# Kernel optimization log

Hardware: AMD Instinct MI355X
Metric: run time of the kernel (lower is better)

## Reference

```python
import jax, jax.numpy as jnp
import numpy as np

BN_EPS = 1e-5


def setup_inputs() -> dict:
    key = jax.random.key(0)
    ks = jax.random.split(key, 6)
    B, C, N = 8, 256, 2048
    C4 = C // 4
    return {
        "x": jax.random.normal(ks[0], (B, C, N), dtype=jnp.float32),
        "wq": jax.random.normal(ks[1], (C4, C), dtype=jnp.float32) * (1.0 / np.sqrt(C)),
        "wv": jax.random.normal(ks[2], (C, C), dtype=jnp.float32) * (1.0 / np.sqrt(C)),
        "bv": jax.random.normal(ks[3], (C,), dtype=jnp.float32) * 0.02,
        "wt": jax.random.normal(ks[4], (C, C), dtype=jnp.float32) * (1.0 / np.sqrt(C)),
        "bt": jax.random.normal(ks[5], (C,), dtype=jnp.float32) * 0.02,
        "gamma": jnp.ones((C,), dtype=jnp.float32),
        "beta": jnp.zeros((C,), dtype=jnp.float32),
    }


def reference(x, wq, wv, bv, wt, bt, gamma, beta):
    # x: [B, C, N]. Conv1d(kernel=1) == per-point matmul.
    # q_conv and k_conv share the same weight in the original, so q == k.
    q = jnp.einsum('oc,bcn->bon', wq, x)            # [B, C/4, N]
    # ||q_i - q_j||_2 via the Gram identity (same math as norm of the diff tensor)
    sq = jnp.sum(q * q, axis=1)                     # [B, N]
    gram = jnp.einsum('bci,bcj->bij', q, q)         # [B, N, N]
    d2 = sq[:, :, None] - 2.0 * gram + sq[:, None, :]
    l2 = jnp.sqrt(jnp.maximum(d2, 0.0))             # [B, N, N]
    attn = jax.nn.softmax(-l2, axis=-1)             # rows = queries i
    v = jnp.einsum('oc,bcn->bon', wv, x) + bv[None, :, None]   # [B, C, N]
    # einsum('bij,bkj->bik') then permute(0,2,1) == contract j directly to [B, C, N]
    x_r = jnp.einsum('bij,bcj->bci', attn, v)       # [B, C, N]
    t = jnp.einsum('oc,bcn->bon', wt, x_r) + bt[None, :, None]
    # BatchNorm1d in training mode: batch stats over (B, N), biased variance
    mean = jnp.mean(t, axis=(0, 2), keepdims=True)
    var = jnp.mean((t - mean) ** 2, axis=(0, 2), keepdims=True)
    bn = gamma[None, :, None] * (t - mean) * jax.lax.rsqrt(var + BN_EPS) + beta[None, :, None]
    return x + jnp.maximum(bn, 0.0)
```

## Files before the change

kernel.cpp:

```cpp
#include <hip/hip_runtime.h>
#include <math.h>

#define BDIM 8
#define CDIM 256
#define C4DIM 64
#define NDIM 2048
#define LOG2E_SQ 2.0813689810056077f
#define NEG_2LOG2E_SQ -4.1627379620112154f

typedef short bf16x8 __attribute__((ext_vector_type(8)));
typedef float f32x4 __attribute__((ext_vector_type(4)));

__device__ inline unsigned cvt_pk(float lo, float hi) {
  unsigned r;
  asm("v_cvt_pk_bf16_f32 %0, %1, %2" : "=v"(r) : "v"(lo), "v"(hi));
  return r;
}
__device__ inline float bflo(unsigned u) {
  u <<= 16; float f; __builtin_memcpy(&f, &u, 4); return f;
}
__device__ inline float bfhi(unsigned u) {
  u &= 0xffff0000u; float f; __builtin_memcpy(&f, &u, 4); return f;
}

__global__ __launch_bounds__(256) void prep_kernel(const float* __restrict__ x,
                                                   const float* __restrict__ wq,
                                                   const float* __restrict__ wv,
                                                   const float* __restrict__ wt,
                                                   short* __restrict__ xT,
                                                   short* __restrict__ xb,
                                                   short* __restrict__ wqb,
                                                   short* __restrict__ wvb,
                                                   short* __restrict__ wtb,
                                                   float* __restrict__ bnsum) {
  __shared__ float tile[64][65];
  const int fb = blockIdx.x, t = threadIdx.x;
  if (fb < 1024) {
    const int b = fb >> 7, c0 = ((fb >> 5) & 3) * 64, n0 = (fb & 31) * 64;
    const int cl = t >> 2, ng = (t & 3) * 16;
#pragma unroll
    for (int kk = 0; kk < 4; ++kk) {
      const size_t src = ((size_t)(b * CDIM + c0 + cl)) * NDIM + n0 + ng + kk * 4;
      float4 v = *(const float4*)&x[src];
      tile[cl][ng + kk * 4 + 0] = v.x; tile[cl][ng + kk * 4 + 1] = v.y;
      tile[cl][ng + kk * 4 + 2] = v.z; tile[cl][ng + kk * 4 + 3] = v.w;
      *(uint2*)&xb[src] = make_uint2(cvt_pk(v.x, v.y), cvt_pk(v.z, v.w));
    }
    __syncthreads();
    const int nl = t >> 2, cg = (t & 3) * 16;
    unsigned u[8];
#pragma unroll
    for (int e = 0; e < 8; ++e)
      u[e] = cvt_pk(tile[cg + 2 * e][nl], tile[cg + 2 * e + 1][nl]);
    short* dst = &xT[((size_t)b * NDIM + n0 + nl) * CDIM + c0 + cg];
    *(uint4*)&dst[0] = make_uint4(u[0], u[1], u[2], u[3]);
    *(uint4*)&dst[8] = make_uint4(u[4], u[5], u[6], u[7]);
  } else if (fb < 1168) {
    const int idx = ((fb - 1024) * 256 + t) * 4;
    const float* src; short* dst; int off;
    if (idx < 16384)      { src = wq; dst = wqb; off = idx; }
    else if (idx < 81920) { src = wv; dst = wvb; off = idx - 16384; }
    else                  { src = wt; dst = wtb; off = idx - 81920; }
    float4 v = *(const float4*)&src[off];
    *(uint2*)&dst[off] = make_uint2(cvt_pk(v.x, v.y), cvt_pk(v.z, v.w));
  } else {
    bnsum[t] = 0.f; bnsum[256 + t] = 0.f;
  }
}

template<bool STATS>
__device__ __forceinline__ void gemm128(const short* __restrict__ Wb,
                                        const short* __restrict__ Xt,
                                        const float* __restrict__ bias,
                                        short* __restrict__ OUT,
                                        float* __restrict__ bnsum,
                                        float* __restrict__ bnss,
                                        int b, int n0, int c0, int t) {
  const int w = t >> 6, l = t & 63, il = l & 15, g = l >> 4;
  const int wn = w & 1, wc = w >> 1;
  const size_t arow = (size_t)b * NDIM + n0 + wn * 64;
  const int ccol = c0 + wc * 64;
  f32x4 acc[4][4] = {};
#pragma unroll
  for (int ks = 0; ks < 8; ++ks) {
    const int k0 = ks * 32;
    bf16x8 af[4], bfr[4];
#pragma unroll
    for (int nt = 0; nt < 4; ++nt)
      af[nt] = *(const bf16x8*)&Xt[(arow + nt * 16 + il) * CDIM + k0 + g * 8];
#pragma unroll
    for (int ct = 0; ct < 4; ++ct)
      bfr[ct] = *(const bf16x8*)&Wb[(size_t)(ccol + ct * 16 + il) * CDIM + k0 + g * 8];
#pragma unroll
    for (int nt = 0; nt < 4; ++nt)
#pragma unroll
      for (int ct = 0; ct < 4; ++ct)
        acc[nt][ct] = __builtin_amdgcn_mfma_f32_16x16x32_bf16(af[nt], bfr[ct], acc[nt][ct], 0, 0, 0);
  }
#pragma unroll
  for (int ct = 0; ct < 4; ++ct) {
    const int c = ccol + ct * 16 + il;
    const float bs = bias[c];
    float s = 0.f, ss = 0.f;
#pragma unroll
    for (int nt = 0; nt < 4; ++nt) {
      const int n = n0 + wn * 64 + nt * 16 + g * 4;
      float y0 = acc[nt][ct][0] + bs, y1 = acc[nt][ct][1] + bs;
      float y2 = acc[nt][ct][2] + bs, y3 = acc[nt][ct][3] + bs;
      *(uint2*)&OUT[((size_t)(b * CDIM + c)) * NDIM + n] =
          make_uint2(cvt_pk(y0, y1), cvt_pk(y2, y3));
      if (STATS) {
        s += y0 + y1 + y2 + y3;
        ss += y0 * y0 + y1 * y1 + y2 * y2 + y3 * y3;
      }
    }
    if (STATS) {
      s += __shfl_xor(s, 16, 64);   s += __shfl_xor(s, 32, 64);
      ss += __shfl_xor(ss, 16, 64); ss += __shfl_xor(ss, 32, 64);
      if (l < 16) { atomicAdd(&bnsum[c], s); atomicAdd(&bnss[c], ss); }
    }
  }
}

__global__ __launch_bounds__(256) void qv_gemm(const short* __restrict__ wqb,
                                               const short* __restrict__ wvb,
                                               const short* __restrict__ xT,
                                               const float* __restrict__ bv,
                                               short* __restrict__ qT,
                                               float* __restrict__ sq2,
                                               short* __restrict__ vbf) {
  const int fb = blockIdx.x, t = threadIdx.x;
  if (fb < 256) {
    const int b = fb >> 5, c0 = ((fb >> 4) & 1) * 128, n0 = (fb & 15) * 128;
    gemm128<false>(wvb, xT, bv, vbf, nullptr, nullptr, b, n0, c0, t);
  } else {
    const int f = fb - 256;
    const int b = f >> 5, n0 = (f & 31) * 64;
    const int w = t >> 6, l = t & 63, il = l & 15, g = l >> 4;
    const int nw = n0 + w * 16;
    f32x4 acc[4] = {};
#pragma unroll
    for (int ks = 0; ks < 8; ++ks) {
      const int k0 = ks * 32;
      bf16x8 bx = *(const bf16x8*)&xT[((size_t)b * NDIM + nw + il) * CDIM + k0 + g * 8];
#pragma unroll
      for (int ot = 0; ot < 4; ++ot) {
        bf16x8 aw = *(const bf16x8*)&wqb[(size_t)(ot * 16 + il) * CDIM + k0 + g * 8];
        acc[ot] = __builtin_amdgcn_mfma_f32_16x16x32_bf16(aw, bx, acc[ot], 0, 0, 0);
      }
    }
    float sqs = 0.f;
#pragma unroll
    for (int ot = 0; ot < 4; ++ot) {
      unsigned u0 = cvt_pk(acc[ot][0], acc[ot][1]);
      unsigned u1 = cvt_pk(acc[ot][2], acc[ot][3]);
      *(uint2*)&qT[((size_t)b * NDIM + nw + il) * C4DIM + ot * 16 + g * 4] = make_uint2(u0, u1);
      float f0 = bflo(u0), f1 = bfhi(u0), f2 = bflo(u1), f3 = bfhi(u1);
      sqs += f0 * f0 + f1 * f1 + f2 * f2 + f3 * f3;
    }
    sqs += __shfl_xor(sqs, 16, 64);
    sqs += __shfl_xor(sqs, 32, 64);
    if (l < 16) sq2[(size_t)b * NDIM + nw + l] = sqs * LOG2E_SQ;
  }
}

__global__ __launch_bounds__(512) void attn_mfma(const short* __restrict__ qT,
                                                 const short* __restrict__ Vb16,
                                                 const float* __restrict__ sq2,
                                                 short* __restrict__ xrT) {
  __shared__ __align__(16) short vj[2][256 * 32];
  __shared__ __align__(16) short qj[2][32 * 64];
  __shared__ __align__(16) short wlds[2][4][16][40];
  __shared__ float sums_lds[8][16];

  const int bid = blockIdx.x;
  const int swz = (bid & 7) * 32 + (bid >> 3);
  const int i0 = (swz & 31) * 64;
  const int b  = swz >> 5;

  const int t = threadIdx.x;
  const int w = t >> 6, l = t & 63, il = l & 15, g = l >> 4;
  const int isub = w & 3, chalf = w >> 2;

  const short* qTb = qT + (size_t)b * NDIM * C4DIM;
  const short* Vbb = Vb16 + (size_t)b * CDIM * NDIM;
  const float* sqb = sq2 + (size_t)b * NDIM;

  const int iglob = i0 + isub * 16 + il;
  const bf16x8 bq0 = *(const bf16x8*)&qTb[(size_t)iglob * C4DIM + g * 8];
  const bf16x8 bq1 = *(const bf16x8*)&qTb[(size_t)iglob * C4DIM + 32 + g * 8];
  const float sqi = sqb[iglob];

  const int vcb = t >> 2, vs = t & 3;
  const int vd0 = vcb * 32 + ((vs ^ ((vcb >> 1) & 3)) << 3);
  const int vd1 = vd0 + 128 * 32;
  const int qrow = t >> 3, qslot = t & 7;
  const int qd = qrow * 64 + ((qslot ^ (qrow & 7)) << 3);

  f32x4 acc[8];
#pragma unroll
  for (int k = 0; k < 8; ++k) acc[k] = {0.f, 0.f, 0.f, 0.f};
  float sumw = 0.f;

  f32x4 sqc;
  {
    if (t < 256) {
      bf16x8 qr = *(const bf16x8*)&qTb[(size_t)qrow * C4DIM + qslot * 8];
      *(bf16x8*)&qj[0][qd] = qr;
    }
    sqc = *(const f32x4*)&sqb[chalf * 16 + g * 4];
  }
  __syncthreads();

  const int NT = NDIM / 32;
  for (int jt = 0; jt <= NT; ++jt) {
    const int p = jt & 1;
    const bool dg = (jt < NT);
    const bool dp = (jt > 0);
    const bool nq = (jt + 1 < NT);

    bf16x8 vr0 = {}, vr1 = {}, qr = {};
    f32x4 tn = {};
    if (dg) {
      const int j0 = jt * 32;
      vr0 = *(const bf16x8*)&Vbb[(size_t)vcb * NDIM + j0 + vs * 8];
      vr1 = *(const bf16x8*)&Vbb[(size_t)(vcb + 128) * NDIM + j0 + vs * 8];
    }
    if (nq) {
      const int j1 = (jt + 1) * 32;
      if (t < 256) qr = *(const bf16x8*)&qTb[(size_t)(j1 + qrow) * C4DIM + qslot * 8];
      tn = *(const f32x4*)&sqb[j1 + chalf * 16 + g * 4];
    }

    f32x4 s = {0.f, 0.f, 0.f, 0.f};
    if (dg) {
      const short* qbuf = &qj[p][0];
      const int row = chalf * 16 + il;
      bf16x8 aJ0 = *(const bf16x8*)&qbuf[row * 64 + ((g ^ (il & 7)) << 3)];
      bf16x8 aJ1 = *(const bf16x8*)&qbuf[row * 64 + (((4 + g) ^ (il & 7)) << 3)];
      s = __builtin_amdgcn_mfma_f32_16x16x32_bf16(aJ0, bq0, s, 0, 0, 0);
      s = __builtin_amdgcn_mfma_f32_16x16x32_bf16(aJ1, bq1, s, 0, 0, 0);
    }

    if (dp) {
      const int pp = p ^ 1;
      const short* vbuf = &vj[pp][0];
      const bf16x8 bw = *(const bf16x8*)&wlds[pp][isub][il][g * 8];
      __builtin_amdgcn_s_setprio(1);
#pragma unroll
      for (int ctl = 0; ctl < 8; ++ctl) {
        const int lr = chalf * 128 + ctl * 16 + il;
        bf16x8 aV = *(const bf16x8*)&vbuf[lr * 32 + ((g ^ ((il >> 1) & 3)) << 3)];
        acc[ctl] = __builtin_amdgcn_mfma_f32_16x16x32_bf16(aV, bw, acc[ctl], 0, 0, 0);
      }
      __builtin_amdgcn_s_setprio(0);
    }

    if (dg) {
      float wv[4];
#pragma unroll
      for (int r = 0; r < 4; ++r) {
        float e = fmaxf(fmaf(NEG_2LOG2E_SQ, s[r], sqi + sqc[r]), 0.f);
        wv[r] = __builtin_amdgcn_exp2f(-__builtin_amdgcn_sqrtf(e));
        sumw += wv[r];
      }
      *(uint2*)&wlds[p][isub][il][chalf * 16 + g * 4] =
          make_uint2(cvt_pk(wv[0], wv[1]), cvt_pk(wv[2], wv[3]));
    }

    if (dg) {
      *(bf16x8*)&vj[p][vd0] = vr0;
      *(bf16x8*)&vj[p][vd1] = vr1;
    }
    if (nq) {
      if (t < 256) *(bf16x8*)&qj[p ^ 1][qd] = qr;
      sqc = tn;
    }
    __syncthreads();
  }

  sumw += __shfl_xor(sumw, 16, 64);
  sumw += __shfl_xor(sumw, 32, 64);
  if (l < 16) sums_lds[w][l] = sumw;
  __syncthreads();
  const float inv = 1.f / (sums_lds[isub][il] + sums_lds[isub + 4][il]);
#pragma unroll
  for (int ctl = 0; ctl < 8; ++ctl) {
    float y0 = acc[ctl][0] * inv, y1 = acc[ctl][1] * inv;
    float y2 = acc[ctl][2] * inv, y3 = acc[ctl][3] * inv;
    *(uint2*)&xrT[((size_t)b * NDIM + iglob) * CDIM + chalf * 128 + ctl * 16 + g * 4] =
        make_uint2(cvt_pk(y0, y1), cvt_pk(y2, y3));
  }
}

__global__ __launch_bounds__(256) void t_gemm(const short* __restrict__ wtb,
                                              const short* __restrict__ xrT,
                                              const float* __restrict__ bt,
                                              short* __restrict__ tbf,
                                              float* __restrict__ bnsum,
                                              float* __restrict__ bnss) {
  gemm128<true>(wtb, xrT, bt, tbf, bnsum, bnss,
                blockIdx.z, blockIdx.x * 128, blockIdx.y * 128, threadIdx.x);
}

__global__ __launch_bounds__(256) void final_kernel(const short* __restrict__ xb,
                                                    const short* __restrict__ tbf,
                                                    const float* __restrict__ bnsum,
                                                    const float* __restrict__ bnss,
                                                    const float* __restrict__ gamma,
                                                    const float* __restrict__ beta,
                                                    float* __restrict__ out) {
  const size_t idx = ((size_t)blockIdx.x * 256 + threadIdx.x) << 2;
  const int c = (int)((idx >> 11) & 255);
  const float cnt = (float)(BDIM * NDIM);
  const float mean = bnsum[c] / cnt;
  const float var = fmaxf(bnss[c] / cnt - mean * mean, 0.f);
  const float sc = gamma[c] * rsqrtf(var + 1e-5f);
  const float sh = beta[c] - mean * sc;
  uint2 xu = *(const uint2*)&xb[idx];
  uint2 tu = *(const uint2*)&tbf[idx];
  const float t0 = bflo(tu.x), t1 = bfhi(tu.x), t2 = bflo(tu.y), t3 = bfhi(tu.y);
  float4 r;
  r.x = bflo(xu.x) + fmaxf(t0 * sc + sh, 0.f);
  r.y = bfhi(xu.x) + fmaxf(t1 * sc + sh, 0.f);
  r.z = bflo(xu.y) + fmaxf(t2 * sc + sh, 0.f);
  r.w = bfhi(xu.y) + fmaxf(t3 * sc + sh, 0.f);
  *(float4*)&out[idx] = r;
}

extern "C" void kernel_launch(void* const* d_in, const int* in_sizes, int n_in,
                              void* d_out, int out_size, void* d_ws, size_t ws_size,
                              hipStream_t stream) {
  const float* x     = (const float*)d_in[0];
  const float* wq    = (const float*)d_in[1];
  const float* wv    = (const float*)d_in[2];
  const float* bv    = (const float*)d_in[3];
  const float* wt    = (const float*)d_in[4];
  const float* bt    = (const float*)d_in[5];
  const float* gamma = (const float*)d_in[6];
  const float* beta  = (const float*)d_in[7];
  float* out = (float*)d_out;
  char* ws = (char*)d_ws;

  short* xbT   = (short*)(ws);
  short* xrT   = xbT;
  short* xb    = (short*)(ws + ((size_t)8  << 20));
  short* wqb   = (short*)(ws + ((size_t)16 << 20));
  short* wvb   = (short*)(ws + ((size_t)16 << 20) + (256 << 10));
  short* wtb   = (short*)(ws + ((size_t)16 << 20) + (512 << 10));
  short* qT    = (short*)(ws + ((size_t)17 << 20));
  float* sq2   = (float*)(ws + ((size_t)19 << 20));
  short* vbf   = (short*)(ws + ((size_t)20 << 20));
  short* tbf   = vbf;
  float* bnsum = (float*)(ws + ((size_t)28 << 20));
  float* bnss  = bnsum + 256;

  prep_kernel<<<dim3(1169), 256, 0, stream>>>(x, wq, wv, wt, xbT, xb, wqb, wvb, wtb, bnsum);
  qv_gemm<<<dim3(512), 256, 0, stream>>>(wqb, wvb, xbT, bv, qT, sq2, vbf);
  attn_mfma<<<dim3(256), 512, 0, stream>>>(qT, vbf, sq2, xrT);
  t_gemm<<<dim3(16, 2, 8), 256, 0, stream>>>(wtb, xrT, bt, tbf, bnsum, bnss);
  final_kernel<<<dim3(4096), 256, 0, stream>>>(xb, tbf, bnsum, bnss, gamma, beta, out);
}
```

Before: 120.4 us.

## Split attention channels across blocks and load V/Q fragments directly from global

The attention kernel now runs 512 blocks of 256 threads, each handling one channel half, instead of 256 blocks of 512 threads that split channels across waves. Each wave computes the full 32-key score tile itself and reads V and Q fragments straight from global memory into registers, which removes the double-buffered shared-memory staging and the per-iteration block barrier. Only a per-wave weight tile stays in shared memory. The cost is that the QK scores and exponentials are computed twice (once per channel half), and V is read from global with strided, less coalesced accesses and no explicit cross-iteration prefetch.

```diff
diff --git a/kernel.cpp b/kernel.cpp
--- a/kernel.cpp
+++ b/kernel.cpp
@@ -164,126 +164,93 @@
   }
 }
 
-__global__ __launch_bounds__(512) void attn_mfma(const short* __restrict__ qT,
+__global__ __launch_bounds__(256) void attn_mfma(const short* __restrict__ qT,
                                                  const short* __restrict__ Vb16,
                                                  const float* __restrict__ sq2,
                                                  short* __restrict__ xrT) {
-  __shared__ __align__(16) short vj[2][256 * 32];
-  __shared__ __align__(16) short qj[2][32 * 64];
-  __shared__ __align__(16) short wlds[2][4][16][40];
-  __shared__ float sums_lds[8][16];
+  __shared__ __align__(16) short wlds[4][16][40];
 
   const int bid = blockIdx.x;
-  const int swz = (bid & 7) * 32 + (bid >> 3);
-  const int i0 = (swz & 31) * 64;
-  const int b  = swz >> 5;
+  const int swz = (bid & 7) * 64 + (bid >> 3);
+  const int i0    = (swz & 31) * 64;
+  const int chalf = (swz >> 5) & 1;
+  const int b     = swz >> 6;
 
   const int t = threadIdx.x;
   const int w = t >> 6, l = t & 63, il = l & 15, g = l >> 4;
-  const int isub = w & 3, chalf = w >> 2;
 
   const short* qTb = qT + (size_t)b * NDIM * C4DIM;
-  const short* Vbb = Vb16 + (size_t)b * CDIM * NDIM;
+  const short* Vbb = Vb16 + ((size_t)b * CDIM + chalf * 128) * NDIM;
   const float* sqb = sq2 + (size_t)b * NDIM;
 
-  const int iglob = i0 + isub * 16 + il;
+  const int iglob = i0 + w * 16 + il;
   const bf16x8 bq0 = *(const bf16x8*)&qTb[(size_t)iglob * C4DIM + g * 8];
   const bf16x8 bq1 = *(const bf16x8*)&qTb[(size_t)iglob * C4DIM + 32 + g * 8];
   const float sqi = sqb[iglob];
 
-  const int vcb = t >> 2, vs = t & 3;
-  const int vd0 = vcb * 32 + ((vs ^ ((vcb >> 1) & 3)) << 3);
-  const int vd1 = vd0 + 128 * 32;
-  const int qrow = t >> 3, qslot = t & 7;
-  const int qd = qrow * 64 + ((qslot ^ (qrow & 7)) << 3);
-
   f32x4 acc[8];
 #pragma unroll
   for (int k = 0; k < 8; ++k) acc[k] = {0.f, 0.f, 0.f, 0.f};
   float sumw = 0.f;
 
-  f32x4 sqc;
-  {
-    if (t < 256) {
-      bf16x8 qr = *(const bf16x8*)&qTb[(size_t)qrow * C4DIM + qslot * 8];
-      *(bf16x8*)&qj[0][qd] = qr;
-    }
-    sqc = *(const f32x4*)&sqb[chalf * 16 + g * 4];
-  }
-  __syncthreads();
+  bf16x8 qfA[2], qfB[2];
+  f32x4 sqc[2];
+#pragma unroll
+  for (int h = 0; h < 2; ++h) {
+    const size_t qr = (size_t)(h * 16 + il) * C4DIM;
+    qfA[h] = *(const bf16x8*)&qTb[qr + g * 8];
+    qfB[h] = *(const bf16x8*)&qTb[qr + 32 + g * 8];
+    sqc[h] = *(const f32x4*)&sqb[h * 16 + g * 4];
+  }
 
   const int NT = NDIM / 32;
-  for (int jt = 0; jt <= NT; ++jt) {
-    const int p = jt & 1;
-    const bool dg = (jt < NT);
-    const bool dp = (jt > 0);
-    const bool nq = (jt + 1 < NT);
-
-    bf16x8 vr0 = {}, vr1 = {}, qr = {};
-    f32x4 tn = {};
-    if (dg) {
-      const int j0 = jt * 32;
-      vr0 = *(const bf16x8*)&Vbb[(size_t)vcb * NDIM + j0 + vs * 8];
-      vr1 = *(const bf16x8*)&Vbb[(size_t)(vcb + 128) * NDIM + j0 + vs * 8];
-    }
-    if (nq) {
-      const int j1 = (jt + 1) * 32;
-      if (t < 256) qr = *(const bf16x8*)&qTb[(size_t)(j1 + qrow) * C4DIM + qslot * 8];
-      tn = *(const f32x4*)&sqb[j1 + chalf * 16 + g * 4];
-    }
-
-    f32x4 s = {0.f, 0.f, 0.f, 0.f};
-    if (dg) {
-      const short* qbuf = &qj[p][0];
-      const int row = chalf * 16 + il;
-      bf16x8 aJ0 = *(const bf16x8*)&qbuf[row * 64 + ((g ^ (il & 7)) << 3)];
-      bf16x8 aJ1 = *(const bf16x8*)&qbuf[row * 64 + (((4 + g) ^ (il & 7)) << 3)];
-      s = __builtin_amdgcn_mfma_f32_16x16x32_bf16(aJ0, bq0, s, 0, 0, 0);
-      s = __builtin_amdgcn_mfma_f32_16x16x32_bf16(aJ1, bq1, s, 0, 0, 0);
-    }
-
-    if (dp) {
-      const int pp = p ^ 1;
-      const short* vbuf = &vj[pp][0];
-      const bf16x8 bw = *(const bf16x8*)&wlds[pp][isub][il][g * 8];
-      __builtin_amdgcn_s_setprio(1);
-#pragma unroll
-      for (int ctl = 0; ctl < 8; ++ctl) {
-        const int lr = chalf * 128 + ctl * 16 + il;
-        bf16x8 aV = *(const bf16x8*)&vbuf[lr * 32 + ((g ^ ((il >> 1) & 3)) << 3)];
-        acc[ctl] = __builtin_amdgcn_mfma_f32_16x16x32_bf16(aV, bw, acc[ctl], 0, 0, 0);
-      }
-      __builtin_amdgcn_s_setprio(0);
-    }
-
-    if (dg) {
+  for (int jt = 0; jt < NT; ++jt) {
+    const int j0 = jt * 32;
+    const bool hn = (jt + 1 < NT);
+
+    bf16x8 va[8];
+#pragma unroll
+    for (int ctl = 0; ctl < 8; ++ctl)
+      va[ctl] = *(const bf16x8*)&Vbb[(size_t)(ctl * 16 + il) * NDIM + j0 + g * 8];
+
+#pragma unroll
+    for (int h = 0; h < 2; ++h) {
+      f32x4 s = {0.f, 0.f, 0.f, 0.f};
+      s = __builtin_amdgcn_mfma_f32_16x16x32_bf16(qfA[h], bq0, s, 0, 0, 0);
+      s = __builtin_amdgcn_mfma_f32_16x16x32_bf16(qfB[h], bq1, s, 0, 0, 0);
       float wv[4];
 #pragma unroll
       for (int r = 0; r < 4; ++r) {
-        float e = fmaxf(fmaf(NEG_2LOG2E_SQ, s[r], sqi + sqc[r]), 0.f);
+        float e = fmaxf(fmaf(NEG_2LOG2E_SQ, s[r], sqi + sqc[h][r]), 0.f);
         wv[r] = __builtin_amdgcn_exp2f(-__builtin_amdgcn_sqrtf(e));
         sumw += wv[r];
       }
-      *(uint2*)&wlds[p][isub][il][chalf * 16 + g * 4] =
+      *(uint2*)&wlds[w][il][h * 16 + g * 4] =
           make_uint2(cvt_pk(wv[0], wv[1]), cvt_pk(wv[2], wv[3]));
     }
 
-    if (dg) {
-      *(bf16x8*)&vj[p][vd0] = vr0;
-      *(bf16x8*)&vj[p][vd1] = vr1;
-    }
-    if (nq) {
-      if (t < 256) *(bf16x8*)&qj[p ^ 1][qd] = qr;
-      sqc = tn;
-    }
-    __syncthreads();
+    if (hn) {
+      const int j1 = j0 + 32;
+#pragma unroll
+      for (int h = 0; h < 2; ++h) {
+        const size_t qr = (size_t)(j1 + h * 16 + il) * C4DIM;
+        qfA[h] = *(const bf16x8*)&qTb[qr + g * 8];
+        qfB[h] = *(const bf16x8*)&qTb[qr + 32 + g * 8];
+        sqc[h] = *(const f32x4*)&sqb[j1 + h * 16 + g * 4];
+      }
+    }
+
+    const bf16x8 bw = *(const bf16x8*)&wlds[w][il][g * 8];
+    __builtin_amdgcn_s_setprio(1);
+#pragma unroll
+    for (int ctl = 0; ctl < 8; ++ctl)
+      acc[ctl] = __builtin_amdgcn_mfma_f32_16x16x32_bf16(va[ctl], bw, acc[ctl], 0, 0, 0);
+    __builtin_amdgcn_s_setprio(0);
   }
 
   sumw += __shfl_xor(sumw, 16, 64);
   sumw += __shfl_xor(sumw, 32, 64);
-  if (l < 16) sums_lds[w][l] = sumw;
-  __syncthreads();
-  const float inv = 1.f / (sums_lds[isub][il] + sums_lds[isub + 4][il]);
+  const float inv = 1.f / sumw;
 #pragma unroll
   for (int ctl = 0; ctl < 8; ++ctl) {
     float y0 = acc[ctl][0] * inv, y1 = acc[ctl][1] * inv;
@@ -357,7 +324,7 @@
 
   prep_kernel<<<dim3(1169), 256, 0, stream>>>(x, wq, wv, wt, xbT, xb, wqb, wvb, wtb, bnsum);
   qv_gemm<<<dim3(512), 256, 0, stream>>>(wqb, wvb, xbT, bv, qT, sq2, vbf);
-  attn_mfma<<<dim3(256), 512, 0, stream>>>(qT, vbf, sq2, xrT);
+  attn_mfma<<<dim3(512), 256, 0, stream>>>(qT, vbf, sq2, xrT);
   t_gemm<<<dim3(16, 2, 8), 256, 0, stream>>>(wtb, xrT, bt, tbf, bnsum, bnss);
   final_kernel<<<dim3(4096), 256, 0, stream>>>(xb, tbf, bnsum, bnss, gamma, beta, out);
 }
```

After: 233.1 us. +93.6%, slower.
